# Kernel tuning notes

Hardware: AMD Instinct MI355X
Metric: run time of the kernel (lower is better)

The kernel has to match this reference:

```python
import jax, jax.numpy as jnp
import numpy as np

INV_SQRT2 = 0.7071067811865476
N, E, K, S = 10000, 120000, 8, 7
DE, DA, DT, DR, DC = 128, 128, 64, 16, 16
T = E * K

def act(x):
    return jax.nn.silu(x)

def residual_stack(x, Ws):
    # Ws: (n_layers, 2, D, D); GemNet ResidualLayer: two Dense+act, scaled skip
    for lw in Ws:
        y = act(act(x @ lw[0]) @ lw[1])
        x = (x + y) * INV_SQRT2
    return x

def bilinear(rbf_W1, sph, m, id_reduce, id_ragged, W):
    # EfficientInteractionBilinear (GemNet): ragged scatter into (E,Kmax,emb) then basis contractions
    m2 = jnp.zeros((rbf_W1.shape[0], sph.shape[1], m.shape[-1]), m.dtype)
    m2 = m2.at[id_reduce, id_ragged].set(m)          # (E, K, DT)
    sum_k = jnp.einsum('eks,ekc->esc', sph, m2)      # (E, S, DT)
    a = jnp.einsum('ejs,esc->ejc', rbf_W1, sum_k)    # (E, DC, DT)
    return jnp.einsum('ejc,cju->eu', a, W)           # (E, DT)

def _forward(h, m_st, rbf_h, rbf3, cbf_rbfW1, cbf_sph,
             W_mlp_st, W_m_kt, W_t_rbf, W_down, W_bil, W_st3, W_ts3,
             res_before, res_after, W_ae_rbf, W_ae_in, res_atom, W_asi, res_m,
             idx_s, idx_t, idx_swap, id3_kt, id3_st, id3_ragged_idx):
    x_skip = m_st @ W_mlp_st
    # --- TripletInteraction ---
    m_kt = act(m_st @ W_m_kt)
    m_kt = m_kt * (rbf3 @ W_t_rbf)        # scale_rbf == 1.0 (identity ScaleFactor)
    m_kt = act(m_kt @ W_down)             # (E, DT)
    xb = bilinear(cbf_rbfW1, cbf_sph, m_kt[id3_kt], id3_st, id3_ragged_idx, W_bil)
    x_st = act(xb @ W_st3)
    x_ts = act(xb @ W_ts3)[idx_swap]
    x3 = (x_st + x_ts) * INV_SQRT2
    # --- merge + residual stacks ---
    x = (x_skip + x3) * INV_SQRT2
    x = residual_stack(x, res_before)
    x = (x + m_st) * INV_SQRT2
    x = residual_stack(x, res_after)
    # --- AtomEmbedding: edge->atom scatter-add ---
    xa = x * (rbf_h @ W_ae_rbf)
    h2 = jax.ops.segment_sum(xa, idx_t, num_segments=h.shape[0])  # scale_sum == 1.0
    h_new = residual_stack(act(h2 @ W_ae_in), res_atom)
    # --- AtomSelfInteraction: gather-concat-Dense ---
    m = act(jnp.concatenate([h_new[idx_s], h_new[idx_t], x], axis=-1) @ W_asi)
    m = residual_stack(m, res_m)
    m = (m + x) * INV_SQRT2
    return h_new, m

def setup_inputs():
    key = jax.random.key(0)
    ks = jax.random.split(key, 24)
    def w(k, shape):
        return jax.random.normal(k, shape, jnp.float32) * (1.0 / np.sqrt(shape[-2]))
    return dict(
        h=jax.random.normal(ks[0], (N, DA), jnp.float32),
        m_st=jax.random.normal(ks[1], (E, DE), jnp.float32),
        rbf_h=jax.random.uniform(ks[2], (E, DR), jnp.float32),
        rbf3=jax.random.uniform(ks[3], (E, DR), jnp.float32),
        cbf_rbfW1=jax.random.normal(ks[4], (E, DC, S), jnp.float32) * 0.2,
        cbf_sph=jax.random.normal(ks[5], (E, K, S), jnp.float32) * 0.2,
        W_mlp_st=w(ks[6], (DE, DE)),
        W_m_kt=w(ks[7], (DE, DE)),
        W_t_rbf=w(ks[8], (DR, DE)),
        W_down=w(ks[9], (DE, DT)),
        W_bil=jax.random.normal(ks[10], (DT, DC, DT), jnp.float32) * (1.0 / np.sqrt(DT * DC)),
        W_st3=w(ks[11], (DT, DE)),
        W_ts3=w(ks[12], (DT, DE)),
        res_before=w(ks[13], (1, 2, DE, DE)),
        res_after=w(ks[14], (2, 2, DE, DE)),
        W_ae_rbf=w(ks[15], (DR, DE)),
        W_ae_in=w(ks[16], (DE, DA)),
        res_atom=w(ks[17], (2, 2, DA, DA)),
        W_asi=w(ks[18], (2 * DA + DE, DE)),
        res_m=w(ks[19], (2, 2, DE, DE)),
        idx_s=jax.random.randint(ks[20], (E,), 0, N, jnp.int32),
        idx_t=jax.random.randint(ks[21], (E,), 0, N, jnp.int32),
        idx_swap=jax.random.permutation(ks[22], E).astype(jnp.int32),
        id3_kt=jax.random.randint(ks[23], (T,), 0, E, jnp.int32),
        id3_st=jnp.repeat(jnp.arange(E, dtype=jnp.int32), K),
        id3_ragged_idx=jnp.tile(jnp.arange(K, dtype=jnp.int32), E),
    )

def reference(h, m_st, rbf_h, rbf3, cbf_rbfW1, cbf_sph,
              W_mlp_st, W_m_kt, W_t_rbf, W_down, W_bil, W_st3, W_ts3,
              res_before, res_after, W_ae_rbf, W_ae_in, res_atom, W_asi, res_m,
              idx_s, idx_t, idx_swap, id3_kt, id3_st, id3_ragged_idx):
    return _forward(h, m_st, rbf_h, rbf3, cbf_rbfW1, cbf_sph,
                    W_mlp_st, W_m_kt, W_t_rbf, W_down, W_bil, W_st3, W_ts3,
                    res_before, res_after, W_ae_rbf, W_ae_in, res_atom, W_asi, res_m,
                    idx_s, idx_t, idx_swap, id3_kt, id3_st, id3_ragged_idx)
```

## Files before the change

### kernel.cpp

```cpp
#include <hip/hip_runtime.h>


#define EE 120000
#define NA 10000

constexpr float C_INV = 0.70710678118654752440f;

using f32x4 = __attribute__((ext_vector_type(4))) float;
using f32x2 = __attribute__((ext_vector_type(2))) float;
using s16x8 = __attribute__((ext_vector_type(8))) short;
using s16x4 = __attribute__((ext_vector_type(4))) short;

__device__ __forceinline__ float act_silu(float x) { return x / (1.0f + __expf(-x)); }

__device__ __forceinline__ unsigned short f2bf(float f) {
    unsigned int u = __float_as_uint(f);
    u += 0x7fffu + ((u >> 16) & 1u);
    return (unsigned short)(u >> 16);
}
__device__ __forceinline__ float bf2f(unsigned short h) {
    return __uint_as_float(((unsigned int)h) << 16);
}
__device__ __forceinline__ unsigned int cvtpk(float a, float b) {
    unsigned int r;
    asm("v_cvt_pk_bf16_f32 %0, %1, %2" : "=v"(r) : "v"(a), "v"(b));
    return r;
}

template<int MT, int KQ>
__device__ __forceinline__ void load_w(const unsigned short* __restrict__ W, int KW,
                                       int l, s16x8 (&a)[MT][KQ])
{
    const int fr = l & 15;
    const int k8 = (l >> 4) << 3;
    #pragma unroll
    for (int mt = 0; mt < MT; ++mt)
        #pragma unroll
        for (int kq = 0; kq < KQ; ++kq)
            a[mt][kq] = *(const s16x8*)&W[(size_t)(mt * 16 + fr) * KW + kq * 32 + k8];
}

template<int MT, int NF, int KQ>
__device__ __forceinline__ void gemm_pre(
    const s16x8 (&a)[MT][KQ], const char* ldsB, int RS,
    int rowBase, int l, f32x4 (&acc)[MT][NF])
{
    const int fr = l & 15;
    const int k8 = (l >> 4) << 3;
    #pragma unroll
    for (int kq = 0; kq < KQ; ++kq) {
        s16x8 b[NF];
        #pragma unroll
        for (int nf = 0; nf < NF; ++nf) {
            const int row = rowBase + nf * 16 + fr;
            const int kb  = ((kq * 32 + k8) * 2) ^ ((row & 7) << 4);
            b[nf] = *(const s16x8*)(ldsB + row * RS + kb);
        }
        #pragma unroll
        for (int mt = 0; mt < MT; ++mt)
            #pragma unroll
            for (int nf = 0; nf < NF; ++nf)
                acc[mt][nf] = __builtin_amdgcn_mfma_f32_16x16x32_bf16(
                    a[mt][kq], b[nf], acc[mt][nf], 0, 0, 0);
    }
}

template<int MT, int NF>
__device__ __forceinline__ void zacc(f32x4 (&acc)[MT][NF])
{
    #pragma unroll
    for (int mt = 0; mt < MT; ++mt)
        #pragma unroll
        for (int nf = 0; nf < NF; ++nf)
            acc[mt][nf] = (f32x4){0.f, 0.f, 0.f, 0.f};
}

__device__ __forceinline__ void packA(char* lds, int RS, int row, int outF0, f32x4 v)
{
    uint2 p;
    p.x = cvtpk(v[0], v[1]);
    p.y = cvtpk(v[2], v[3]);
    *(uint2*)(lds + row * RS + ((outF0 * 2) ^ ((row & 7) << 4))) = p;
}

__device__ __forceinline__ void store_bf4(unsigned short* dst, f32x4 v)
{
    uint2 p;
    p.x = cvtpk(v[0], v[1]);
    p.y = cvtpk(v[2], v[3]);
    *(uint2*)dst = p;
}

template<int ROWS>
__device__ __forceinline__ void stage_f32(char* lds, const float* __restrict__ src,
                                          int row0, int M, int tid)
{
    #pragma unroll
    for (int u = 0; u < ROWS * 16 / 512; ++u) {
        const int flat = tid + u * 512;
        const int row  = flat >> 4;
        const int k8   = (flat & 15) << 3;
        const int grow = row0 + row;
        uint4 val = {0u, 0u, 0u, 0u};
        if (grow < M) {
            const float* p = src + (size_t)grow * 128 + k8;
            f32x4 lo = *(const f32x4*)p;
            f32x4 hi = *(const f32x4*)(p + 4);
            val.x = cvtpk(lo[0], lo[1]);
            val.y = cvtpk(lo[2], lo[3]);
            val.z = cvtpk(hi[0], hi[1]);
            val.w = cvtpk(hi[2], hi[3]);
        }
        *(uint4*)(lds + row * 256 + ((k8 * 2) ^ ((row & 7) << 4))) = val;
    }
}

template<bool MSTM, int NF>
__device__ __forceinline__ void res_layer(
    char* A, char* B,
    const unsigned short* W0, const unsigned short* W1,
    int wm, int wn, int l, f32x4 (&x)[2][NF],
    const s16x4 (*ms)[NF])
{
    const int fr = l & 15;
    const int fq = (l >> 4) << 2;

    s16x8 aw[2][4];
    load_w<2, 4>(W0 + (size_t)(wm * 32) * 128, 128, l, aw);
    f32x4 acc[2][NF];
    zacc(acc);
    gemm_pre<2, NF, 4>(aw, A, 256, wn * NF * 16, l, acc);

    s16x8 aw1[2][4];
    load_w<2, 4>(W1 + (size_t)(wm * 32) * 128, 128, l, aw1);

    #pragma unroll
    for (int mt = 0; mt < 2; ++mt)
        #pragma unroll
        for (int nf = 0; nf < NF; ++nf) {
            const int row = wn * NF * 16 + nf * 16 + fr;
            const int of0 = wm * 32 + mt * 16 + fq;
            f32x4 v;
            #pragma unroll
            for (int q = 0; q < 4; ++q) v[q] = act_silu(acc[mt][nf][q]);
            packA(B, 256, row, of0, v);
        }
    __syncthreads();

    zacc(acc);
    gemm_pre<2, NF, 4>(aw1, B, 256, wn * NF * 16, l, acc);
    #pragma unroll
    for (int mt = 0; mt < 2; ++mt)
        #pragma unroll
        for (int nf = 0; nf < NF; ++nf) {
            const int row = wn * NF * 16 + nf * 16 + fr;
            const int of0 = wm * 32 + mt * 16 + fq;
            #pragma unroll
            for (int q = 0; q < 4; ++q)
                x[mt][nf][q] = (x[mt][nf][q] + act_silu(acc[mt][nf][q])) * C_INV;
            if (MSTM) {
                #pragma unroll
                for (int q = 0; q < 4; ++q)
                    x[mt][nf][q] = (x[mt][nf][q] +
                                    bf2f((unsigned short)ms[mt][nf][q])) * C_INV;
            }
            packA(A, 256, row, of0, x[mt][nf]);
        }
    __syncthreads();
}

__device__ __forceinline__ s16x4 read_frag(const char* lds, int row, int of0)
{
    return *(const s16x4*)(lds + row * 256 + ((of0 * 2) ^ ((row & 7) << 4)));
}

__global__ __launch_bounds__(512, 4) void front_k(
    const float* __restrict__ m_st, const unsigned short* __restrict__ scale_b,
    const unsigned short* __restrict__ Wmkt, const unsigned short* __restrict__ Wdown,
    unsigned short* __restrict__ mkt_b)
{
    __shared__ char A[128 * 256];
    const int tid = threadIdx.x;
    const int l = tid & 63, w = tid >> 6, wm = w & 3, wn = w >> 2;
    const int fr = l & 15, fq = (l >> 4) << 2;
    const int row0 = blockIdx.x * 128;

    s16x8 aw[2][4];
    load_w<2, 4>(Wmkt + (size_t)(wm * 32) * 128, 128, l, aw);

    stage_f32<128>(A, m_st, row0, EE, tid);
    __syncthreads();

    f32x4 acc[2][4];
    zacc(acc);
    gemm_pre<2, 4, 4>(aw, A, 256, wn * 64, l, acc);

    s16x8 aw2[1][4];
    load_w<1, 4>(Wdown + (size_t)(wm * 16) * 128, 128, l, aw2);

    __syncthreads();
    #pragma unroll
    for (int mt = 0; mt < 2; ++mt)
        #pragma unroll
        for (int nf = 0; nf < 4; ++nf) {
            const int row = wn * 64 + nf * 16 + fr;
            const int grow = row0 + row;
            const int of0 = wm * 32 + mt * 16 + fq;
            f32x4 v = {0.f, 0.f, 0.f, 0.f};
            if (grow < EE) {
                s16x4 sc = *(const s16x4*)&scale_b[(size_t)grow * 128 + of0];
                #pragma unroll
                for (int q = 0; q < 4; ++q)
                    v[q] = act_silu(acc[mt][nf][q]) * bf2f((unsigned short)sc[q]);
            }
            packA(A, 256, row, of0, v);
        }
    __syncthreads();

    f32x4 acc2[1][4];
    zacc(acc2);
    gemm_pre<1, 4, 4>(aw2, A, 256, wn * 64, l, acc2);
    #pragma unroll
    for (int nf = 0; nf < 4; ++nf) {
        const int row = wn * 64 + nf * 16 + fr;
        const int grow = row0 + row;
        if (grow >= EE) continue;
        const int of0 = wm * 16 + fq;
        f32x4 v;
        #pragma unroll
        for (int q = 0; q < 4; ++q) v[q] = act_silu(acc2[0][nf][q]);
        store_bf4(&mkt_b[(size_t)grow * 64 + of0], v);
    }
}

__global__ __launch_bounds__(512, 4) void chain_k(
    const float* __restrict__ m_st,
    const unsigned short* __restrict__ yst, const unsigned short* __restrict__ yts,
    const int* __restrict__ idx_swap,
    const unsigned short* __restrict__ Wmlp,
    const unsigned short* __restrict__ Wrb0, const unsigned short* __restrict__ Wrb1,
    const unsigned short* __restrict__ Wra0, const unsigned short* __restrict__ Wra1,
    const unsigned short* __restrict__ Wra2, const unsigned short* __restrict__ Wra3,
    unsigned short* __restrict__ xb_out)
{
    __shared__ char A[128 * 256];
    __shared__ char B[128 * 256];
    const int tid = threadIdx.x;
    const int l = tid & 63, w = tid >> 6, wm = w & 3, wn = w >> 2;
    const int fr = l & 15, fq = (l >> 4) << 2;
    const int row0 = blockIdx.x * 128;

    s16x8 aw[2][4];
    load_w<2, 4>(Wmlp + (size_t)(wm * 32) * 128, 128, l, aw);

    stage_f32<128>(A, m_st, row0, EE, tid);
    __syncthreads();

    f32x4 acc[2][4];
    zacc(acc);
    gemm_pre<2, 4, 4>(aw, A, 256, wn * 64, l, acc);

    s16x4 ms[2][4];
    #pragma unroll
    for (int mt = 0; mt < 2; ++mt)
        #pragma unroll
        for (int nf = 0; nf < 4; ++nf)
            ms[mt][nf] = read_frag(A, wn * 64 + nf * 16 + fr, wm * 32 + mt * 16 + fq);

    f32x4 x[2][4];
    #pragma unroll
    for (int mt = 0; mt < 2; ++mt)
        #pragma unroll
        for (int nf = 0; nf < 4; ++nf) {
            const int row = wn * 64 + nf * 16 + fr;
            const int grow = row0 + row;
            const int of0 = wm * 32 + mt * 16 + fq;
            if (grow < EE) {
                s16x4 a = *(const s16x4*)&yst[(size_t)grow * 128 + of0];
                const int sw = idx_swap[grow];
                s16x4 b = *(const s16x4*)&yts[(size_t)sw * 128 + of0];
                #pragma unroll
                for (int q = 0; q < 4; ++q)
                    x[mt][nf][q] = (acc[mt][nf][q] +
                        (bf2f((unsigned short)a[q]) + bf2f((unsigned short)b[q])) * C_INV) * C_INV;
            } else {
                x[mt][nf] = (f32x4){0.f, 0.f, 0.f, 0.f};
            }
        }
    __syncthreads();
    #pragma unroll
    for (int mt = 0; mt < 2; ++mt)
        #pragma unroll
        for (int nf = 0; nf < 4; ++nf)
            packA(A, 256, wn * 64 + nf * 16 + fr, wm * 32 + mt * 16 + fq, x[mt][nf]);
    __syncthreads();

    res_layer<true , 4>(A, B, Wrb0, Wrb1, wm, wn, l, x, ms);
    res_layer<false, 4>(A, B, Wra0, Wra1, wm, wn, l, x, nullptr);
    res_layer<false, 4>(A, B, Wra2, Wra3, wm, wn, l, x, nullptr);

    #pragma unroll
    for (int mt = 0; mt < 2; ++mt)
        #pragma unroll
        for (int nf = 0; nf < 4; ++nf) {
            const int row = wn * 64 + nf * 16 + fr;
            const int grow = row0 + row;
            if (grow >= EE) continue;
            const int of0 = wm * 32 + mt * 16 + fq;
            store_bf4(&xb_out[(size_t)grow * 128 + of0], x[mt][nf]);
        }
}

__global__ __launch_bounds__(512, 4) void atom_k(
    const float* __restrict__ h2,
    const unsigned short* __restrict__ Wae,
    const unsigned short* __restrict__ Wr0, const unsigned short* __restrict__ Wr1,
    const unsigned short* __restrict__ Wr2, const unsigned short* __restrict__ Wr3,
    float* __restrict__ out_h, unsigned short* __restrict__ h_b)
{
    __shared__ char A[64 * 256];
    __shared__ char B[64 * 256];
    const int tid = threadIdx.x;
    const int l = tid & 63, w = tid >> 6, wm = w & 3, wn = w >> 2;
    const int fr = l & 15, fq = (l >> 4) << 2;
    const int row0 = blockIdx.x * 64;

    s16x8 aw[2][4];
    load_w<2, 4>(Wae + (size_t)(wm * 32) * 128, 128, l, aw);

    stage_f32<64>(A, h2, row0, NA, tid);
    __syncthreads();

    f32x4 acc[2][2];
    zacc(acc);
    gemm_pre<2, 2, 4>(aw, A, 256, wn * 32, l, acc);
    f32x4 x[2][2];
    #pragma unroll
    for (int mt = 0; mt < 2; ++mt)
        #pragma unroll
        for (int nf = 0; nf < 2; ++nf)
            #pragma unroll
            for (int q = 0; q < 4; ++q)
                x[mt][nf][q] = act_silu(acc[mt][nf][q]);
    __syncthreads();
    #pragma unroll
    for (int mt = 0; mt < 2; ++mt)
        #pragma unroll
        for (int nf = 0; nf < 2; ++nf)
            packA(A, 256, wn * 32 + nf * 16 + fr, wm * 32 + mt * 16 + fq, x[mt][nf]);
    __syncthreads();

    res_layer<false, 2>(A, B, Wr0, Wr1, wm, wn, l, x, nullptr);
    res_layer<false, 2>(A, B, Wr2, Wr3, wm, wn, l, x, nullptr);

    #pragma unroll
    for (int mt = 0; mt < 2; ++mt)
        #pragma unroll
        for (int nf = 0; nf < 2; ++nf) {
            const int row = wn * 32 + nf * 16 + fr;
            const int grow = row0 + row;
            if (grow >= NA) continue;
            const int of0 = wm * 32 + mt * 16 + fq;
            *(f32x4*)&out_h[(size_t)grow * 128 + of0] = x[mt][nf];
            store_bf4(&h_b[(size_t)grow * 128 + of0], x[mt][nf]);
        }
}

__global__ __launch_bounds__(512, 4) void asi_k(
    const unsigned short* __restrict__ h_b, const unsigned short* __restrict__ x_b,
    const int* __restrict__ idx_s, const int* __restrict__ idx_t,
    const unsigned short* __restrict__ Wasi,
    const unsigned short* __restrict__ Wm0, const unsigned short* __restrict__ Wm1,
    const unsigned short* __restrict__ Wm2, const unsigned short* __restrict__ Wm3,
    float* __restrict__ out_m)
{
    __shared__ char A[128 * 256];
    __shared__ char B[128 * 256];
    const int tid = threadIdx.x;
    const int l = tid & 63, w = tid >> 6, wm = w & 3, wn = w >> 2;
    const int fr = l & 15, fq = (l >> 4) << 2;
    const int row0 = blockIdx.x * 128;

    f32x4 acc[2][4];
    zacc(acc);

    for (int c = 0; c < 3; ++c) {
        s16x8 aw[2][4];
        load_w<2, 4>(Wasi + (size_t)(wm * 32) * 384 + c * 128, 384, l, aw);
        #pragma unroll
        for (int u = 0; u < 4; ++u) {
            const int flat = tid + u * 512;
            const int row = flat >> 4;
            const int k8 = (flat & 15) << 3;
            const int grow = row0 + row;
            s16x8 v = {0, 0, 0, 0, 0, 0, 0, 0};
            if (grow < EE) {
                const unsigned short* src =
                    (c == 0) ? h_b + (size_t)idx_s[grow] * 128
                  : (c == 1) ? h_b + (size_t)idx_t[grow] * 128
                             : x_b + (size_t)grow * 128;
                v = *(const s16x8*)&src[k8];
            }
            *(s16x8*)(A + row * 256 + ((k8 * 2) ^ ((row & 7) << 4))) = v;
        }
        __syncthreads();
        gemm_pre<2, 4, 4>(aw, A, 256, wn * 64, l, acc);
        __syncthreads();
    }

    f32x4 x[2][4];
    #pragma unroll
    for (int mt = 0; mt < 2; ++mt)
        #pragma unroll
        for (int nf = 0; nf < 4; ++nf)
            #pragma unroll
            for (int q = 0; q < 4; ++q)
                x[mt][nf][q] = act_silu(acc[mt][nf][q]);
    #pragma unroll
    for (int mt = 0; mt < 2; ++mt)
        #pragma unroll
        for (int nf = 0; nf < 4; ++nf)
            packA(A, 256, wn * 64 + nf * 16 + fr, wm * 32 + mt * 16 + fq, x[mt][nf]);
    __syncthreads();

    res_layer<false, 4>(A, B, Wm0, Wm1, wm, wn, l, x, nullptr);
    res_layer<false, 4>(A, B, Wm2, Wm3, wm, wn, l, x, nullptr);

    #pragma unroll
    for (int mt = 0; mt < 2; ++mt)
        #pragma unroll
        for (int nf = 0; nf < 4; ++nf) {
            const int row = wn * 64 + nf * 16 + fr;
            const int grow = row0 + row;
            if (grow >= EE) continue;
            const int of0 = wm * 32 + mt * 16 + fq;
            s16x4 xv = *(const s16x4*)&x_b[(size_t)grow * 128 + of0];
            f32x4 o;
            #pragma unroll
            for (int q = 0; q < 4; ++q)
                o[q] = (x[mt][nf][q] + bf2f((unsigned short)xv[q])) * C_INV;
            *(f32x4*)&out_m[(size_t)grow * 128 + of0] = o;
        }
}

__global__ __launch_bounds__(256) void rbf_scale_k(
    const float* __restrict__ A, const float* __restrict__ W,
    unsigned short* __restrict__ out, int M)
{
    __shared__ float Ws[16][128];
    const int tid = threadIdx.x;
    #pragma unroll
    for (int t = tid; t < 512; t += 256) {
        int kk = t >> 5, c4 = (t & 31) << 2;
        *(float4*)&Ws[kk][c4] = *(const float4*)(W + kk * 128 + c4);
    }
    __syncthreads();
    const int tx = tid & 31, ty = tid >> 5;
    const int row0 = blockIdx.x * 128;
    #pragma unroll
    for (int i = 0; i < 16; ++i) {
        const int row = row0 + ty + i * 8;
        if (row >= M) continue;
        float av[16];
        #pragma unroll
        for (int j = 0; j < 4; ++j) {
            float4 a = *(const float4*)(A + (size_t)row * 16 + j * 4);
            av[j * 4] = a.x; av[j * 4 + 1] = a.y; av[j * 4 + 2] = a.z; av[j * 4 + 3] = a.w;
        }
        f32x4 s = {0.f, 0.f, 0.f, 0.f};
        #pragma unroll
        for (int k = 0; k < 16; ++k) {
            float4 wv = *(const float4*)&Ws[k][tx * 4];
            s[0] += av[k] * wv.x; s[1] += av[k] * wv.y;
            s[2] += av[k] * wv.z; s[3] += av[k] * wv.w;
        }
        store_bf4(&out[(size_t)row * 128 + tx * 4], s);
    }
}

__global__ void hist_k(const int* __restrict__ idxt, int* __restrict__ cnt)
{
    int i = blockIdx.x * 256 + threadIdx.x;
    if (i < EE) atomicAdd(&cnt[idxt[i]], 1);
}

__global__ __launch_bounds__(256) void scan_k(const int* __restrict__ cnt,
                                              int* __restrict__ start, int* __restrict__ wrk)
{
    __shared__ int ps[256];
    const int t = threadIdx.x;
    int s = 0;
    for (int j = 0; j < 40; ++j) {
        int idx = t * 40 + j;
        if (idx < NA) s += cnt[idx];
    }
    ps[t] = s;
    __syncthreads();
    for (int off = 1; off < 256; off <<= 1) {
        int v = (t >= off) ? ps[t - off] : 0;
        __syncthreads();
        ps[t] += v;
        __syncthreads();
    }
    int run = ps[t] - s;
    for (int j = 0; j < 40; ++j) {
        int idx = t * 40 + j;
        if (idx < NA) {
            start[idx] = run;
            wrk[idx] = run;
            run += cnt[idx];
        }
    }
    if (t == 255) start[NA] = ps[255];
}

__global__ void place_k(const int* __restrict__ idxt, int* __restrict__ wrk,
                        int* __restrict__ order)
{
    int i = blockIdx.x * 256 + threadIdx.x;
    if (i < EE) {
        int pos = atomicAdd(&wrk[idxt[i]], 1);
        order[pos] = i;
    }
}

__global__ __launch_bounds__(256) void segsum_k(
    const unsigned short* __restrict__ x_b, const float* __restrict__ rbf_h,
    const float* __restrict__ Wae, const int* __restrict__ start,
    const int* __restrict__ order, float* __restrict__ h2)
{
    const int tid = threadIdx.x;
    const int l = tid & 63, w = tid >> 6;
    const int a = blockIdx.x * 4 + w;
    if (a >= NA) return;

    float wc[32];
    #pragma unroll
    for (int j = 0; j < 16; ++j) {
        f32x2 v = *(const f32x2*)(Wae + j * 128 + 2 * l);
        wc[2 * j] = v[0]; wc[2 * j + 1] = v[1];
    }

    const int s = start[a], e_end = start[a + 1];
    float acc0 = 0.f, acc1 = 0.f;
    for (int i = s; i < e_end; ++i) {
        const int e = __builtin_amdgcn_readfirstlane(order[i]);
        const unsigned int xv = *(const unsigned int*)(x_b + (size_t)e * 128 + 2 * l);
        const float* rp = rbf_h + (size_t)e * 16;
        float c0 = 0.f, c1 = 0.f;
        #pragma unroll
        for (int j = 0; j < 16; ++j) {
            float r = rp[j];
            c0 += r * wc[2 * j];
            c1 += r * wc[2 * j + 1];
        }
        acc0 += bf2f((unsigned short)(xv & 0xffff)) * c0;
        acc1 += bf2f((unsigned short)(xv >> 16)) * c1;
    }
    f32x2 o; o[0] = acc0; o[1] = acc1;
    *(f32x2*)&h2[(size_t)a * 128 + 2 * l] = o;
}

__global__ void wconv_k(const float* __restrict__ Wbil, unsigned short* __restrict__ WT)
{
    int t = blockIdx.x * 256 + threadIdx.x;
    int u = t >> 10, k = t & 1023, j = k >> 6, c = k & 63;
    WT[t] = f2bf(Wbil[(size_t)(c * 16 + j) * 64 + u]);
}

struct WDesc { const float* src; int K; int N; int off; };
struct WTab  { WDesc d[21]; };

__global__ void wconvall_k(WTab tab, unsigned short* __restrict__ dst)
{
    WDesc d = tab.d[blockIdx.x];
    const int tot = d.K * d.N;
    for (int i = threadIdx.x; i < tot; i += 256) {
        int n = i / d.K, k = i - n * d.K;
        dst[d.off + i] = f2bf(d.src[(size_t)k * d.N + n]);
    }
}

__device__ __forceinline__ float rlc(const f32x4& cv, int idx, int lbase)
{
    const int c = idx & 3;
    float comp = (c == 0) ? cv[0] : (c == 1) ? cv[1] : (c == 2) ? cv[2] : cv[3];
    return __uint_as_float(__builtin_amdgcn_readlane(__float_as_uint(comp),
                                                     lbase + (idx >> 2)));
}

__device__ __forceinline__ void bl_stage(
    const float* __restrict__ sph, const float* __restrict__ rbfW1,
    const int* __restrict__ id3kt, int eG, int l,
    f32x4& cv, int (&ids)[8])
{
    cv = (f32x4){0.f, 0.f, 0.f, 0.f};
    if (l < 14)       cv = *(const f32x4*)(sph   + (size_t)eG * 56  + l * 4);
    else if (l < 42)  cv = *(const f32x4*)(rbfW1 + (size_t)eG * 112 + (l - 14) * 4);
    #pragma unroll
    for (int k = 0; k < 8; ++k) ids[k] = id3kt[eG * 8 + k];
}

__device__ __forceinline__ void bl_gather(
    const unsigned short* __restrict__ mkt, const int (&ids)[8], int l,
    unsigned int (&m2)[8])
{
    #pragma unroll
    for (int k = 0; k < 8; ++k)
        m2[k] = mkt[(size_t)ids[k] * 64 + l];
}

__device__ __forceinline__ void bl_compute(
    const f32x4& cv, const unsigned int (&m2)[8],
    unsigned short* __restrict__ aS, int eL, int l)
{
    float sk[7] = {0.f, 0.f, 0.f, 0.f, 0.f, 0.f, 0.f};
    #pragma unroll
    for (int k = 0; k < 8; ++k) {
        const float mv = __uint_as_float(m2[k] << 16);
        #pragma unroll
        for (int s = 0; s < 7; ++s)
            sk[s] += rlc(cv, k * 7 + s, 0) * mv;
    }
    unsigned short* arow = aS + eL * 1024;
    const int lsw = l ^ ((eL & 7) << 3);
    #pragma unroll
    for (int j = 0; j < 16; ++j) {
        float av = 0.f;
        #pragma unroll
        for (int s = 0; s < 7; ++s)
            av += rlc(cv, j * 7 + s, 14) * sk[s];
        arow[j * 64 + lsw] = f2bf(av);
    }
}

__global__ __launch_bounds__(512) void bilinear7_k(
    const unsigned short* __restrict__ mkt,
    const float* __restrict__ rbfW1,
    const float* __restrict__ sph,
    const int*   __restrict__ id3kt,
    const unsigned short* __restrict__ WT,
    const unsigned short* __restrict__ Wst3,
    const unsigned short* __restrict__ Wts3,
    unsigned short* __restrict__ yst,
    unsigned short* __restrict__ yts)
{
    __shared__ unsigned short aS[32 * 1024];
    float* pS = (float*)aS;

    const int tid = threadIdx.x;
    const int l   = tid & 63;
    const int w   = tid >> 6;
    const int e0  = blockIdx.x * 32;
    const int fr  = l & 15;
    const int fq  = (l >> 4) << 2;

    s16x8 bfrag[4][4];
    {
        const int u  = l & 15;
        const int kh = w * 128 + ((l >> 4) << 3);
        #pragma unroll
        for (int nt = 0; nt < 4; ++nt)
            #pragma unroll
            for (int kq = 0; kq < 4; ++kq)
                bfrag[nt][kq] = *(const s16x8*)&WT[(size_t)(nt * 16 + u) * 1024 + kh + kq * 32];
    }

    f32x4 cv0, cv1, cv2, cv3;
    int  id0[8], id1[8], id2[8], id3[8];
    unsigned int m0[8], m1[8], m2v[8], m3[8];

    bl_stage(sph, rbfW1, id3kt, e0 + 0 * 8 + w, l, cv0, id0);
    bl_stage(sph, rbfW1, id3kt, e0 + 1 * 8 + w, l, cv1, id1);
    bl_gather(mkt, id0, l, m0);
    bl_gather(mkt, id1, l, m1);
    bl_stage(sph, rbfW1, id3kt, e0 + 2 * 8 + w, l, cv2, id2);
    bl_compute(cv0, m0, aS, 0 * 8 + w, l);
    bl_gather(mkt, id2, l, m2v);
    bl_stage(sph, rbfW1, id3kt, e0 + 3 * 8 + w, l, cv3, id3);
    bl_compute(cv1, m1, aS, 1 * 8 + w, l);
    bl_gather(mkt, id3, l, m3);
    bl_compute(cv2, m2v, aS, 2 * 8 + w, l);
    bl_compute(cv3, m3, aS, 3 * 8 + w, l);
    __syncthreads();

    f32x4 acc[2][4];
    #pragma unroll
    for (int mt = 0; mt < 2; ++mt)
        #pragma unroll
        for (int nt = 0; nt < 4; ++nt)
            acc[mt][nt] = (f32x4){0.f, 0.f, 0.f, 0.f};

    const int kbase = w * 128 + ((l >> 4) << 3);
    #pragma unroll
    for (int kq = 0; kq < 4; ++kq) {
        s16x8 afr[2];
        #pragma unroll
        for (int mt = 0; mt < 2; ++mt) {
            const int row = mt * 16 + (l & 15);
            const int kk  = (kbase + kq * 32) ^ ((row & 7) << 3);
            afr[mt] = *(const s16x8*)&aS[row * 1024 + kk];
        }
        #pragma unroll
        for (int mt = 0; mt < 2; ++mt)
            #pragma unroll
            for (int nt = 0; nt < 4; ++nt)
                acc[mt][nt] = __builtin_amdgcn_mfma_f32_16x16x32_bf16(
                    afr[mt], bfrag[nt][kq], acc[mt][nt], 0, 0, 0);
    }
    __syncthreads();

    #pragma unroll
    for (int mt = 0; mt < 2; ++mt)
        #pragma unroll
        for (int nt = 0; nt < 4; ++nt)
            #pragma unroll
            for (int q = 0; q < 4; ++q) {
                const int e = mt * 16 + ((l >> 4) << 2) + q;
                const int u = nt * 16 + (l & 15);
                pS[(w * 32 + e) * 64 + u] = acc[mt][nt][q];
            }
    __syncthreads();

    f32x4 s;
    {
        const int e  = tid >> 4;
        const int u0 = (tid & 15) << 2;
        s = (f32x4){0.f, 0.f, 0.f, 0.f};
        #pragma unroll
        for (int ww = 0; ww < 8; ++ww)
            s += *(const f32x4*)&pS[(ww * 32 + e) * 64 + u0];
    }
    __syncthreads();

    unsigned short* xbS = aS;
    {
        const int e  = tid >> 4;
        const int u0 = (tid & 15) << 2;
        uint2 p;
        p.x = cvtpk(s[0], s[1]);
        p.y = cvtpk(s[2], s[3]);
        *(uint2*)((char*)xbS + e * 128 + ((u0 * 2) ^ ((e & 7) << 4))) = p;
    }
    __syncthreads();

    const unsigned short* Wsel = (w < 4) ? Wst3 : Wts3;
    unsigned short*       ysel = (w < 4) ? yst : yts;
    const int wmF = w & 3;

    s16x8 awF[2][2];
    load_w<2, 2>(Wsel + (size_t)(wmF * 32) * 64, 64, l, awF);
    f32x4 accF[2][2];
    zacc(accF);
    gemm_pre<2, 2, 2>(awF, (const char*)xbS, 128, 0, l, accF);

    #pragma unroll
    for (int mt = 0; mt < 2; ++mt)
        #pragma unroll
        for (int nf = 0; nf < 2; ++nf) {
            const int row = nf * 16 + fr;
            const int of0 = wmF * 32 + mt * 16 + fq;
            f32x4 v;
            #pragma unroll
            for (int q = 0; q < 4; ++q) v[q] = act_silu(accF[mt][nf][q]);
            store_bf4(&ysel[(size_t)(e0 + row) * 128 + of0], v);
        }
}

extern "C" void kernel_launch(void* const* d_in, const int* in_sizes, int n_in,
                              void* d_out, int out_size, void* d_ws, size_t ws_size,
                              hipStream_t stream)
{
    const float* m_st      = (const float*)d_in[1];
    const float* rbf_h     = (const float*)d_in[2];
    const float* rbf3      = (const float*)d_in[3];
    const float* cbf_rbfW1 = (const float*)d_in[4];
    const float* cbf_sph   = (const float*)d_in[5];
    const float* W_mlp_st  = (const float*)d_in[6];
    const float* W_m_kt    = (const float*)d_in[7];
    const float* W_t_rbf   = (const float*)d_in[8];
    const float* W_down    = (const float*)d_in[9];
    const float* W_bil     = (const float*)d_in[10];
    const float* W_st3     = (const float*)d_in[11];
    const float* W_ts3     = (const float*)d_in[12];
    const float* resb      = (const float*)d_in[13];
    const float* resa      = (const float*)d_in[14];
    const float* W_ae_rbf  = (const float*)d_in[15];
    const float* W_ae_in   = (const float*)d_in[16];
    const float* resat     = (const float*)d_in[17];
    const float* W_asi     = (const float*)d_in[18];
    const float* resm      = (const float*)d_in[19];
    const int*   idx_s     = (const int*)d_in[20];
    const int*   idx_t     = (const int*)d_in[21];
    const int*   idx_swap  = (const int*)d_in[22];
    const int*   id3_kt    = (const int*)d_in[23];

    float* h2 = (float*)d_ws;
    unsigned short* scale_b = (unsigned short*)(h2 + (size_t)NA * 128);
    unsigned short* yst_b   = scale_b;
    unsigned short* yts_b   = scale_b + (size_t)EE * 128;
    unsigned short* x_b     = yts_b + (size_t)EE * 128;
    unsigned short* mkt_b   = x_b + (size_t)EE * 128;
    unsigned short* xb_b    = mkt_b + (size_t)EE * 64;
    unsigned short* h_b     = xb_b + (size_t)EE * 64;
    unsigned short* WTbil   = h_b + (size_t)NA * 128;
    unsigned short* WTall   = WTbil + 65536;
    int* cnt   = (int*)(WTall + 352256);
    int* start = cnt + NA;
    int* wrk   = start + NA + 1;
    int* order = wrk + NA;

    float* out_h = (float*)d_out;
    float* out_m = out_h + (size_t)NA * 128;

    const dim3 blk(256);
    const dim3 blk5(512);
    const int gE  = (EE + 127) / 128;
    const int gN64 = (NA + 63) / 64;
    constexpr size_t SQ = 128 * 128;

    WTab tab; int off = 0; int oi = 0;
    auto put = [&](const float* s, int K, int N) {
        int o = off; tab.d[oi].src = s; tab.d[oi].K = K; tab.d[oi].N = N;
        tab.d[oi].off = o; ++oi; off += K * N; return o;
    };
    const int o_mlp  = put(W_mlp_st, 128, 128);
    const int o_mktw = put(W_m_kt, 128, 128);
    const int o_down = put(W_down, 128, 64);
    const int o_st3  = put(W_st3, 64, 128);
    const int o_ts3  = put(W_ts3, 64, 128);
    const int o_rb0  = put(resb, 128, 128);
    const int o_rb1  = put(resb + SQ, 128, 128);
    const int o_ra0  = put(resa, 128, 128);
    const int o_ra1  = put(resa + SQ, 128, 128);
    const int o_ra2  = put(resa + 2 * SQ, 128, 128);
    const int o_ra3  = put(resa + 3 * SQ, 128, 128);
    const int o_aein = put(W_ae_in, 128, 128);
    const int o_rat0 = put(resat, 128, 128);
    const int o_rat1 = put(resat + SQ, 128, 128);
    const int o_rat2 = put(resat + 2 * SQ, 128, 128);
    const int o_rat3 = put(resat + 3 * SQ, 128, 128);
    const int o_asi  = put(W_asi, 384, 128);
    const int o_rm0  = put(resm, 128, 128);
    const int o_rm1  = put(resm + SQ, 128, 128);
    const int o_rm2  = put(resm + 2 * SQ, 128, 128);
    const int o_rm3  = put(resm + 3 * SQ, 128, 128);

    hipMemsetAsync(cnt, 0, NA * sizeof(int), stream);
    wconv_k<<<65536 / 256, blk, 0, stream>>>(W_bil, WTbil);
    wconvall_k<<<21, blk, 0, stream>>>(tab, WTall);
    hist_k<<<(EE + 255) / 256, blk, 0, stream>>>(idx_t, cnt);
    scan_k<<<1, blk, 0, stream>>>(cnt, start, wrk);
    place_k<<<(EE + 255) / 256, blk, 0, stream>>>(idx_t, wrk, order);

    rbf_scale_k<<<gE, blk, 0, stream>>>(rbf3, W_t_rbf, scale_b, EE);
    front_k<<<gE, blk5, 0, stream>>>(m_st, scale_b, WTall + o_mktw, WTall + o_down, mkt_b);
    bilinear7_k<<<EE / 32, blk5, 0, stream>>>(
        mkt_b, cbf_rbfW1, cbf_sph, id3_kt, WTbil,
        WTall + o_st3, WTall + o_ts3, yst_b, yts_b);
    chain_k<<<gE, blk5, 0, stream>>>(
        m_st, yst_b, yts_b, idx_swap,
        WTall + o_mlp, WTall + o_rb0, WTall + o_rb1,
        WTall + o_ra0, WTall + o_ra1, WTall + o_ra2, WTall + o_ra3,
        x_b);
    segsum_k<<<(NA + 3) / 4, blk, 0, stream>>>(x_b, rbf_h, W_ae_rbf, start, order, h2);
    atom_k<<<gN64, blk5, 0, stream>>>(
        h2, WTall + o_aein,
        WTall + o_rat0, WTall + o_rat1, WTall + o_rat2, WTall + o_rat3,
        out_h, h_b);
    asi_k<<<gE, blk5, 0, stream>>>(
        h_b, x_b, idx_s, idx_t,
        WTall + o_asi,
        WTall + o_rm0, WTall + o_rm1, WTall + o_rm2, WTall + o_rm3,
        out_m);
}
```

Baseline: 669.0 us.

## Precompute per-edge rbf·sph coefficient matrix in shared memory for bilinear

Reassociates the bilinear contraction. A combined (16x8) coefficient C = rbfW1·sph is built per edge, using sph/rbfW1 tiles staged into shared memory. Each lane then computes each of the 16 outputs as an 8-term dot product instead of running two 7-term contraction stages through readlane broadcasts. The per-stage interleaving of loads and compute is replaced by issuing all id and gather loads up front. This adds extra shared memory (Cs, 16KB) and two more block barriers, which may lower occupancy, and raises register pressure from holding all gathered values at once.

```diff
diff --git a/kernel.cpp b/kernel.cpp
--- a/kernel.cpp
+++ b/kernel.cpp
@@ -581,60 +581,7 @@
     }
 }
 
-__device__ __forceinline__ float rlc(const f32x4& cv, int idx, int lbase)
-{
-    const int c = idx & 3;
-    float comp = (c == 0) ? cv[0] : (c == 1) ? cv[1] : (c == 2) ? cv[2] : cv[3];
-    return __uint_as_float(__builtin_amdgcn_readlane(__float_as_uint(comp),
-                                                     lbase + (idx >> 2)));
-}
-
-__device__ __forceinline__ void bl_stage(
-    const float* __restrict__ sph, const float* __restrict__ rbfW1,
-    const int* __restrict__ id3kt, int eG, int l,
-    f32x4& cv, int (&ids)[8])
-{
-    cv = (f32x4){0.f, 0.f, 0.f, 0.f};
-    if (l < 14)       cv = *(const f32x4*)(sph   + (size_t)eG * 56  + l * 4);
-    else if (l < 42)  cv = *(const f32x4*)(rbfW1 + (size_t)eG * 112 + (l - 14) * 4);
-    #pragma unroll
-    for (int k = 0; k < 8; ++k) ids[k] = id3kt[eG * 8 + k];
-}
-
-__device__ __forceinline__ void bl_gather(
-    const unsigned short* __restrict__ mkt, const int (&ids)[8], int l,
-    unsigned int (&m2)[8])
-{
-    #pragma unroll
-    for (int k = 0; k < 8; ++k)
-        m2[k] = mkt[(size_t)ids[k] * 64 + l];
-}
-
-__device__ __forceinline__ void bl_compute(
-    const f32x4& cv, const unsigned int (&m2)[8],
-    unsigned short* __restrict__ aS, int eL, int l)
-{
-    float sk[7] = {0.f, 0.f, 0.f, 0.f, 0.f, 0.f, 0.f};
-    #pragma unroll
-    for (int k = 0; k < 8; ++k) {
-        const float mv = __uint_as_float(m2[k] << 16);
-        #pragma unroll
-        for (int s = 0; s < 7; ++s)
-            sk[s] += rlc(cv, k * 7 + s, 0) * mv;
-    }
-    unsigned short* arow = aS + eL * 1024;
-    const int lsw = l ^ ((eL & 7) << 3);
-    #pragma unroll
-    for (int j = 0; j < 16; ++j) {
-        float av = 0.f;
-        #pragma unroll
-        for (int s = 0; s < 7; ++s)
-            av += rlc(cv, j * 7 + s, 14) * sk[s];
-        arow[j * 64 + lsw] = f2bf(av);
-    }
-}
-
-__global__ __launch_bounds__(512) void bilinear7_k(
+__global__ __launch_bounds__(512) void bilinear8_k(
     const unsigned short* __restrict__ mkt,
     const float* __restrict__ rbfW1,
     const float* __restrict__ sph,
@@ -646,7 +593,10 @@
     unsigned short* __restrict__ yts)
 {
     __shared__ unsigned short aS[32 * 1024];
+    __shared__ float Cs[32 * 128];
     float* pS = (float*)aS;
+    float* sphS = (float*)(aS + 16384);
+    float* rbS  = sphS + 32 * 56;
 
     const int tid = threadIdx.x;
     const int l   = tid & 63;
@@ -655,6 +605,74 @@
     const int fr  = l & 15;
     const int fq  = (l >> 4) << 2;
 
+    {
+        const f32x4* sg = (const f32x4*)(sph + (size_t)e0 * 56);
+        for (int u = tid; u < 448; u += 512) ((f32x4*)sphS)[u] = sg[u];
+        const f32x4* rg = (const f32x4*)(rbfW1 + (size_t)e0 * 112);
+        for (int u = tid; u < 896; u += 512) ((f32x4*)rbS)[u] = rg[u];
+    }
+
+    int ids[4][8];
+    #pragma unroll
+    for (int r = 0; r < 4; ++r) {
+        const int eG = e0 + r * 8 + w;
+        #pragma unroll
+        for (int k = 0; k < 8; ++k) ids[r][k] = id3kt[eG * 8 + k];
+    }
+    unsigned int m0[8], m1[8], m2v[8], m3[8];
+    #pragma unroll
+    for (int k = 0; k < 8; ++k) m0[k] = mkt[(size_t)ids[0][k] * 64 + l];
+    #pragma unroll
+    for (int k = 0; k < 8; ++k) m1[k] = mkt[(size_t)ids[1][k] * 64 + l];
+    #pragma unroll
+    for (int k = 0; k < 8; ++k) m2v[k] = mkt[(size_t)ids[2][k] * 64 + l];
+    #pragma unroll
+    for (int k = 0; k < 8; ++k) m3[k] = mkt[(size_t)ids[3][k] * 64 + l];
+
+    __syncthreads();
+
+    {
+        const int e = tid >> 4;
+        const int j = tid & 15;
+        float rb[7];
+        #pragma unroll
+        for (int s = 0; s < 7; ++s) rb[s] = rbS[e * 112 + j * 7 + s];
+        float cr[8];
+        #pragma unroll
+        for (int k = 0; k < 8; ++k) {
+            float a = 0.f;
+            #pragma unroll
+            for (int s = 0; s < 7; ++s)
+                a += rb[s] * sphS[e * 56 + k * 7 + s];
+            cr[k] = a;
+        }
+        f32x4 lo = {cr[0], cr[1], cr[2], cr[3]};
+        f32x4 hi = {cr[4], cr[5], cr[6], cr[7]};
+        *(f32x4*)&Cs[e * 128 + j * 8]     = lo;
+        *(f32x4*)&Cs[e * 128 + j * 8 + 4] = hi;
+    }
+    __syncthreads();
+
+    #pragma unroll
+    for (int r = 0; r < 4; ++r) {
+        const int eL = r * 8 + w;
+        const float* Ce = &Cs[eL * 128];
+        const unsigned int* mm = (r == 0) ? m0 : (r == 1) ? m1 : (r == 2) ? m2v : m3;
+        float mv[8];
+        #pragma unroll
+        for (int k = 0; k < 8; ++k) mv[k] = __uint_as_float(mm[k] << 16);
+        unsigned short* arow = aS + eL * 1024;
+        const int lsw = l ^ ((eL & 7) << 3);
+        #pragma unroll
+        for (int j = 0; j < 16; ++j) {
+            f32x4 c0 = *(const f32x4*)&Ce[j * 8];
+            f32x4 c1 = *(const f32x4*)&Ce[j * 8 + 4];
+            float av = c0[0] * mv[0] + c0[1] * mv[1] + c0[2] * mv[2] + c0[3] * mv[3]
+                     + c1[0] * mv[4] + c1[1] * mv[5] + c1[2] * mv[6] + c1[3] * mv[7];
+            arow[j * 64 + lsw] = f2bf(av);
+        }
+    }
+
     s16x8 bfrag[4][4];
     {
         const int u  = l & 15;
@@ -665,23 +683,6 @@
             for (int kq = 0; kq < 4; ++kq)
                 bfrag[nt][kq] = *(const s16x8*)&WT[(size_t)(nt * 16 + u) * 1024 + kh + kq * 32];
     }
-
-    f32x4 cv0, cv1, cv2, cv3;
-    int  id0[8], id1[8], id2[8], id3[8];
-    unsigned int m0[8], m1[8], m2v[8], m3[8];
-
-    bl_stage(sph, rbfW1, id3kt, e0 + 0 * 8 + w, l, cv0, id0);
-    bl_stage(sph, rbfW1, id3kt, e0 + 1 * 8 + w, l, cv1, id1);
-    bl_gather(mkt, id0, l, m0);
-    bl_gather(mkt, id1, l, m1);
-    bl_stage(sph, rbfW1, id3kt, e0 + 2 * 8 + w, l, cv2, id2);
-    bl_compute(cv0, m0, aS, 0 * 8 + w, l);
-    bl_gather(mkt, id2, l, m2v);
-    bl_stage(sph, rbfW1, id3kt, e0 + 3 * 8 + w, l, cv3, id3);
-    bl_compute(cv1, m1, aS, 1 * 8 + w, l);
-    bl_gather(mkt, id3, l, m3);
-    bl_compute(cv2, m2v, aS, 2 * 8 + w, l);
-    bl_compute(cv3, m3, aS, 3 * 8 + w, l);
     __syncthreads();
 
     f32x4 acc[2][4];
@@ -855,7 +856,7 @@
 
     rbf_scale_k<<<gE, blk, 0, stream>>>(rbf3, W_t_rbf, scale_b, EE);
     front_k<<<gE, blk5, 0, stream>>>(m_st, scale_b, WTall + o_mktw, WTall + o_down, mkt_b);
-    bilinear7_k<<<EE / 32, blk5, 0, stream>>>(
+    bilinear8_k<<<EE / 32, blk5, 0, stream>>>(
         mkt_b, cbf_rbfW1, cbf_sph, id3_kt, WTbil,
         WTall + o_st3, WTall + o_ts3, yst_b, yts_b);
     chain_k<<<gE, blk5, 0, stream>>>(
```

Result: faster. 629.1 us (-6.0%).
